# Kernel optimization log

Measured on AMD Instinct MI355X. Metric: run time of the kernel, lower is better.

## Reference

```python
import jax, jax.numpy as jnp
import numpy as np

# dims
T, INPUT_DIM = 128, 512
C_INT, ISQ, DIM, C = 8, 16, 256, 8  # internal_channels, input_square_dim, dim, n_channel
OSQ, OUT_CH = 8, 16                  # output_square_dim, output_size // osq^2
INPUT_SCALE, S1, S2 = 1.0, 0.9, 0.1
K1, D1, K2, D2 = 3, 1, 5, 2


def dw_circ_conv(x, w, dilation):
    """Depthwise conv with circular padding. x: [B,C,H,W], w: [C,1,k,k]."""
    k = w.shape[-1]
    pad = dilation * (k - 1) // 2
    xp = jnp.pad(x, ((0, 0), (0, 0), (pad, pad), (pad, pad)), mode='wrap')
    return jax.lax.conv_general_dilated(
        xp, w, window_strides=(1, 1), padding='VALID',
        rhs_dilation=(dilation, dilation), feature_group_count=x.shape[1])


def setup_inputs() -> dict:
    key = jax.random.key(0)
    ks = jax.random.split(key, 10)
    X = jax.random.normal(ks[0], (T, INPUT_DIM), jnp.float32)
    # nn.Linear weight [out, in]
    W_embed = jax.random.normal(ks[1], (C_INT * ISQ * ISQ, INPUT_DIM), jnp.float32) * 0.02
    mask_coarse = jax.random.bernoulli(ks[2], 0.5, (1, 1, ISQ, ISQ)).astype(jnp.float32)
    mask_fine = jax.random.bernoulli(ks[3], 0.5, (1, 1, DIM, DIM)).astype(jnp.float32)
    # ConvTranspose2d weight [in_ch, out_ch, k, k], k = dim // isq = 16
    W_deconv = jax.random.normal(ks[4], (C_INT, C, DIM // ISQ, DIM // ISQ), jnp.float32) * 0.02

    def lateral_w(k, ksz, p):
        # LateralConnections with conn_exp=1: |w| * bernoulli(p), normalized per output channel
        w = jnp.abs(jax.random.normal(k, (C, 1, ksz, ksz), jnp.float32))
        m = jax.random.bernoulli(jax.random.fold_in(k, 1), p, w.shape).astype(jnp.float32)
        w = w * m
        return w / w.sum(axis=(1, 2, 3), keepdims=True)

    w1 = lateral_w(ks[5], K1, 0.9)
    w2 = lateral_w(ks[6], K2, 0.9)
    # output Conv2d: [out_ch, in_ch, k, k], k = dim // osq = 32
    w_out = jax.random.normal(ks[7], (OUT_CH, C, DIM // OSQ, DIM // OSQ), jnp.float32) * 0.01
    b_out = jax.random.normal(ks[8], (OUT_CH,), jnp.float32) * 0.01
    return dict(X=X, W_embed=W_embed, mask_coarse=mask_coarse, mask_fine=mask_fine,
                W_deconv=W_deconv, w1=w1, w2=w2, w_out=w_out, b_out=b_out)


def reference(X, W_embed, mask_coarse, mask_fine, W_deconv, w1, w2, w_out, b_out):
    t = X.shape[0]
    ksz = W_deconv.shape[-1]
    # CorticalInput
    u = (X @ W_embed.T).reshape(t, C_INT, ISQ, ISQ) * mask_coarse  # [T,Cint,isq,isq]
    # ConvTranspose2d with stride == kernel_size (non-overlapping) == block expansion
    u = jnp.einsum('tcij,coab->toiajb', u, W_deconv).reshape(t, C, ISQ * ksz, ISQ * ksz)
    u = INPUT_SCALE * u * mask_fine  # [T,C,dim,dim]

    # sequential reservoir scan
    def step(Z, x):
        Z = jnp.tanh(S1 * dw_circ_conv(Z, w1, D1) + S2 * dw_circ_conv(Z, w2, D2) + x)
        return Z, Z[0]

    Z0 = jnp.zeros((1, C, DIM, DIM), X.dtype)
    _, outs = jax.lax.scan(step, Z0, u)  # outs: [T,C,dim,dim]

    # readout conv (kernel == stride == dim // osq)
    ko = w_out.shape[-1]
    y = jax.lax.conv_general_dilated(outs, w_out, (ko, ko), 'VALID')
    y = y + b_out[None, :, None, None]
    return y.reshape(t, -1)
```

## Files before the change

### kernel.cpp

```cpp
#include <hip/hip_runtime.h>
#include <math.h>

#define SB_OFF   0
#define E_OFF    524288

typedef float vf4 __attribute__((ext_vector_type(4)));

__device__ __forceinline__ float fast_tanh(float x) {
  x = fminf(fmaxf(x, -15.f), 15.f);
  float ex = __expf(2.f * x);
  return __fdividef(ex - 1.f, ex + 1.f);
}

template <int CTRL>
__device__ __forceinline__ float dpp_add(float v) {
  int x = __builtin_amdgcn_update_dpp(0, __float_as_int(v), CTRL, 0xF, 0xF, true);
  return v + __int_as_float(x);
}

__device__ __forceinline__ void st16(float* p, float a, float b, float c, float d) {
  vf4 v; v.x = a; v.y = b; v.z = c; v.w = d;
  asm volatile("global_store_dwordx4 %0, %1, off sc0 sc1" :: "v"(p), "v"(v) : "memory");
}
__device__ __forceinline__ vf4 ld16(const float* p) {
  vf4 r;
  asm volatile("global_load_dwordx4 %0, %1, off sc0 sc1\n"
               "s_waitcnt vmcnt(0)"
               : "=&v"(r) : "v"(p) : "memory");
  return r;
}
__device__ __forceinline__ void tag_store(unsigned* p, unsigned v) {
  asm volatile("s_waitcnt vmcnt(0)\n"
               "global_store_dword %0, %1, off sc0 sc1" :: "v"(p), "v"(v) : "memory");
}

__global__ __launch_bounds__(256) void prep_kernel(
    const float* __restrict__ X, const float* __restrict__ W_embed,
    const float* __restrict__ mask_coarse, const float* __restrict__ b_out,
    float* __restrict__ ws, float* __restrict__ out)
{
  __shared__ float Xl[128][36];
  __shared__ float Wl[8][36];

  const int tid = threadIdx.x, bid = blockIdx.x;
  float* eb = ws + E_OFF;

  {
    int idx = bid * 512 + tid * 2;
    out[idx]     = b_out[(idx >> 6) & 15];
    out[idx + 1] = b_out[((idx + 1) >> 6) & 15];
  }

  const int o0 = bid * 8;
  const int ol = tid & 7;
  const int tg = tid >> 3;
  float acc[4] = {0.f, 0.f, 0.f, 0.f};

  for (int k0 = 0; k0 < 512; k0 += 32) {
    __syncthreads();
#pragma unroll
    for (int p = 0; p < 4; ++p) {
      int tr = p * 32 + (tid >> 3);
      int kc = (tid & 7) * 4;
      *(float4*)&Xl[tr][kc] = *(const float4*)&X[(size_t)tr * 512 + k0 + kc];
    }
    if (tid < 64) {
      int wr = tid >> 3, wc = (tid & 7) * 4;
      *(float4*)&Wl[wr][wc] = *(const float4*)&W_embed[(size_t)(o0 + wr) * 512 + k0 + wc];
    }
    __syncthreads();
#pragma unroll
    for (int kk = 0; kk < 8; ++kk) {
      float4 w4 = *(const float4*)&Wl[ol][kk * 4];
#pragma unroll
      for (int i = 0; i < 4; ++i) {
        float4 x4 = *(const float4*)&Xl[tg * 4 + i][kk * 4];
        acc[i] = fmaf(w4.x, x4.x, fmaf(w4.y, x4.y, fmaf(w4.z, x4.z, fmaf(w4.w, x4.w, acc[i]))));
      }
    }
  }
  const int o = o0 + ol;
  float mc = mask_coarse[o & 255];
#pragma unroll
  for (int i = 0; i < 4; ++i)
    eb[(size_t)(tg * 4 + i) * 2048 + o] = acc[i] * mc;
}

__global__ __launch_bounds__(512, 2) void scan_kernel(
    const float* __restrict__ mask_fine, const float* __restrict__ W_deconv,
    const float* __restrict__ w1, const float* __restrict__ w2,
    const float* __restrict__ w_out, float* __restrict__ ws,
    float* __restrict__ out)
{
  __shared__ float zin[2][72 * 44];
  __shared__ float rowbuf[2][64 * 17];

  const int tid  = threadIdx.x;
  const int bid  = blockIdx.x;
  const int ch   = bid >> 5;
  const int tile = bid & 31;
  const int tI = tile >> 3, tJ = tile & 7;
  const int r0 = tI << 6, c0 = tJ << 5;
  const int row = tid >> 3;
  const int cg  = tid & 7;
  const int lc  = cg << 2;

  float* Zb = ws + SB_OFF;
  const float* eb = ws + E_OFF;
  const int myoff = (ch * 32 + tile) << 10;

  const int i0 = (r0 + row) >> 4;
  const int jj = (c0 + lc) >> 4;
  float4 wd[8];
#pragma unroll
  for (int c = 0; c < 8; ++c)
    wd[c] = *(const float4*)&W_deconv[(((c * 8 + ch) * 16) + (row & 15)) * 16 + (lc & 15)];
  float4 mf = *(const float4*)&mask_fine[(size_t)(r0 + row) * 256 + c0 + lc];
  float4 wo[16];
#pragma unroll
  for (int oc = 0; oc < 16; ++oc)
    wo[oc] = *(const float4*)&w_out[(((oc * 8 + ch) * 32) + (row & 31)) * 32 + lc];
  float w1s[9], w2s[25];
#pragma unroll
  for (int k = 0; k < 9; ++k)
    w1s[k] = __uint_as_float(__builtin_amdgcn_readfirstlane(__float_as_uint(w1[ch * 9 + k])));
#pragma unroll
  for (int k = 0; k < 25; ++k)
    w2s[k] = __uint_as_float(__builtin_amdgcn_readfirstlane(__float_as_uint(w2[ch * 25 + k])));

  int rd_src = 0, rd_dst = 0, rd_tag = 0;
  const bool hasrd = (tid < 208);
  if (hasrd) {
    int u = tid, di = 0, dj = 0, src = 0, dst = 0, wv = 0;
    if (u < 32) {
      di = -1; src = 128 + (u >> 3) * 32 + (u & 7) * 4;
      dst = (u >> 3) * 44 + 4 + (u & 7) * 4; wv = 7;
    } else if (u < 64) {
      int v = u - 32; di = 1; src = (v >> 3) * 32 + (v & 7) * 4;
      dst = (68 + (v >> 3)) * 44 + 4 + (v & 7) * 4; wv = 0;
    } else if (u < 128) {
      int v = u - 64; dj = -1; src = 512 + v * 4; dst = (4 + v) * 44; wv = v >> 3;
    } else if (u < 192) {
      int v = u - 128; dj = 1; src = 256 + v * 4; dst = (4 + v) * 44 + 36; wv = v >> 3;
    } else {
      int v = u - 192, c = v >> 2, r = v & 3;
      if (c == 0)      { di = -1; dj = -1; src = 816 + r * 4; dst = r * 44;            wv = 7; }
      else if (c == 1) { di = -1; dj = 1;  src = 800 + r * 4; dst = r * 44 + 36;       wv = 7; }
      else if (c == 2) { di = 1;  dj = -1; src = 784 + r * 4; dst = (68 + r) * 44;     wv = 0; }
      else             { di = 1;  dj = 1;  src = 768 + r * 4; dst = (68 + r) * 44 + 36; wv = 0; }
    }
    int nI = (tI + di) & 3, nJ = (tJ + dj) & 7;
    int roff = (ch * 32 + nI * 8 + nJ) << 10;
    rd_src = roff + src;
    rd_tag = roff + 832 + wv * 16;
    rd_dst = dst;
  }

  for (int k = tid; k < 2 * 72 * 44; k += 512) zin[0][k] = 0.f;
  __syncthreads();

  for (int t = 0; t < 128; ++t) {
    float* sb = Zb + (size_t)((t + 1) & 1) * 262144;
    const float* zr = zin[t & 1];
    float*       zw = zin[(t + 1) & 1];
    float*       rb = rowbuf[t & 1];

    float ev[8];
#pragma unroll
    for (int c = 0; c < 8; ++c)
      ev[c] = eb[(size_t)t * 2048 + c * 256 + i0 * 16 + jj];

    float c1a[4] = {0, 0, 0, 0}, c2a[4] = {0, 0, 0, 0};
    {
      float w[12];
      auto load_row = [&](int zrr) {
        float4 A  = *(const float4*)&zr[zrr * 44 + lc];
        float4 B  = *(const float4*)&zr[zrr * 44 + lc + 4];
        float4 Cq = *(const float4*)&zr[zrr * 44 + lc + 8];
        w[0]=A.x; w[1]=A.y; w[2]=A.z; w[3]=A.w;
        w[4]=B.x; w[5]=B.y; w[6]=B.z; w[7]=B.w;
        w[8]=Cq.x; w[9]=Cq.y; w[10]=Cq.z; w[11]=Cq.w;
      };
      auto k2row = [&](int a) {
#pragma unroll
        for (int j = 0; j < 4; ++j)
#pragma unroll
          for (int b = 0; b < 5; ++b)
            c2a[j] = fmaf(w[j + 2 * b], w2s[a * 5 + b], c2a[j]);
      };
      auto k1row = [&](int a) {
#pragma unroll
        for (int j = 0; j < 4; ++j)
#pragma unroll
          for (int b = 0; b < 3; ++b)
            c1a[j] = fmaf(w[j + 3 + b], w1s[a * 3 + b], c1a[j]);
      };
      load_row(row + 0); k2row(0);
      load_row(row + 2); k2row(1);
      load_row(row + 3); k1row(0);
      load_row(row + 4); k1row(1); k2row(2);
      load_row(row + 5); k1row(2);
      load_row(row + 6); k2row(3);
      load_row(row + 8); k2row(4);
    }
    float zv[4];
    {
      const float* mfp = (const float*)&mf;
#pragma unroll
      for (int j = 0; j < 4; ++j) {
        float u = 0.f;
#pragma unroll
        for (int c = 0; c < 8; ++c)
          u = fmaf(ev[c], ((const float*)&wd[c])[j], u);
        float val = fmaf(0.9f, c1a[j], fmaf(0.1f, c2a[j], mfp[j] * u));
        zv[j] = fast_tanh(val);
      }
    }

    if (t < 127) {
      float* rec = sb + myoff;
      if (row < 4)   st16(rec + row * 32 + lc, zv[0], zv[1], zv[2], zv[3]);
      if (row >= 60) st16(rec + 128 + (row - 60) * 32 + lc, zv[0], zv[1], zv[2], zv[3]);
      if (lc == 0)   st16(rec + 256 + row * 4, zv[0], zv[1], zv[2], zv[3]);
      if (lc == 28)  st16(rec + 512 + row * 4, zv[0], zv[1], zv[2], zv[3]);
      if (row < 4 && lc == 0)   st16(rec + 768 + row * 4, zv[0], zv[1], zv[2], zv[3]);
      if (row < 4 && lc == 28)  st16(rec + 784 + row * 4, zv[0], zv[1], zv[2], zv[3]);
      if (row >= 60 && lc == 0) st16(rec + 800 + (row - 60) * 4, zv[0], zv[1], zv[2], zv[3]);
      if (row >= 60 && lc == 28) st16(rec + 816 + (row - 60) * 4, zv[0], zv[1], zv[2], zv[3]);
      if ((tid & 63) == 0)
        tag_store((unsigned*)(rec + 832 + (tid >> 6) * 16), (unsigned)(t + 1));
    }

    *(float4*)&zw[(4 + row) * 44 + 4 + lc] = make_float4(zv[0], zv[1], zv[2], zv[3]);

    float racc[16];
#pragma unroll
    for (int oc = 0; oc < 16; ++oc) {
      const float* wop = (const float*)&wo[oc];
      racc[oc] = fmaf(zv[0], wop[0], fmaf(zv[1], wop[1], fmaf(zv[2], wop[2], zv[3] * wop[3])));
    }
#pragma unroll
    for (int k = 0; k < 16; ++k) {
      racc[k] = dpp_add<0xB1>(racc[k]);
      racc[k] = dpp_add<0x4E>(racc[k]);
      racc[k] = dpp_add<0x141>(racc[k]);
    }
    rb[row * 17 + (cg << 1)]     = racc[cg << 1];
    rb[row * 17 + (cg << 1) + 1] = racc[(cg << 1) + 1];

    if (t < 127 && hasrd) {
      const unsigned tg = (unsigned)(t + 1);
      const unsigned* ta = (const unsigned*)(sb + rd_tag);
      int spins = 0;
      while (__hip_atomic_load(ta, __ATOMIC_RELAXED, __HIP_MEMORY_SCOPE_AGENT) != tg) {
        __builtin_amdgcn_s_sleep(1);
        if (++spins > (1 << 18)) break;
      }
      vf4 v = ld16(sb + rd_src);
      zw[rd_dst]     = v.x;
      zw[rd_dst + 1] = v.y;
      zw[rd_dst + 2] = v.z;
      zw[rd_dst + 3] = v.w;
    }

    __syncthreads();

    if (tid < 32) {
      int p = tid >> 4, oc = tid & 15;
      float s = 0.f;
#pragma unroll
      for (int r = 0; r < 32; ++r) s += rb[(p * 32 + r) * 17 + oc];
      atomicAdd(&out[t * 1024 + oc * 64 + (2 * tI + p) * 8 + tJ], s);
    }
  }
}

extern "C" void kernel_launch(void* const* d_in, const int* in_sizes, int n_in,
                              void* d_out, int out_size, void* d_ws, size_t ws_size,
                              hipStream_t stream) {
  const float* X           = (const float*)d_in[0];
  const float* W_embed     = (const float*)d_in[1];
  const float* mask_coarse = (const float*)d_in[2];
  const float* mask_fine   = (const float*)d_in[3];
  const float* W_deconv    = (const float*)d_in[4];
  const float* w1          = (const float*)d_in[5];
  const float* w2          = (const float*)d_in[6];
  const float* w_out       = (const float*)d_in[7];
  const float* b_out       = (const float*)d_in[8];
  float* ws  = (float*)d_ws;
  float* out = (float*)d_out;

  prep_kernel<<<dim3(256), dim3(256), 0, stream>>>(X, W_embed, mask_coarse, b_out, ws, out);
  scan_kernel<<<dim3(256), dim3(512), 0, stream>>>(mask_fine, W_deconv, w1, w2, w_out, ws, out);
}
```

Baseline: 508.0 us.

## Fuse embedding GEMM prep into scan kernel with a global tag barrier

Removes the separate prep kernel and computes the input-embedding GEMM and bias initialisation at the start of the scan kernel. All blocks then synchronise through per-block tags in workspace before the reservoir scan begins. This is meant to save one kernel launch and the gap between the two kernels. It adds shared memory per block and a spin barrier. The tags are never reset to zero, so on a repeated call the barrier may pass before the embedding data is written.

```diff
diff --git a/kernel.cpp b/kernel.cpp
--- a/kernel.cpp
+++ b/kernel.cpp
@@ -3,6 +3,7 @@
 
 #define SB_OFF   0
 #define E_OFF    524288
+#define PT_OFF   786432
 
 typedef float vf4 __attribute__((ext_vector_type(4)));
 
@@ -21,6 +22,9 @@
 __device__ __forceinline__ void st16(float* p, float a, float b, float c, float d) {
   vf4 v; v.x = a; v.y = b; v.z = c; v.w = d;
   asm volatile("global_store_dwordx4 %0, %1, off sc0 sc1" :: "v"(p), "v"(v) : "memory");
+}
+__device__ __forceinline__ void stc(float* p, float v) {
+  asm volatile("global_store_dword %0, %1, off sc0 sc1" :: "v"(p), "v"(v) : "memory");
 }
 __device__ __forceinline__ vf4 ld16(const float* p) {
   vf4 r;
@@ -34,59 +38,9 @@
                "global_store_dword %0, %1, off sc0 sc1" :: "v"(p), "v"(v) : "memory");
 }
 
-__global__ __launch_bounds__(256) void prep_kernel(
+__global__ __launch_bounds__(512, 2) void scan_kernel(
     const float* __restrict__ X, const float* __restrict__ W_embed,
     const float* __restrict__ mask_coarse, const float* __restrict__ b_out,
-    float* __restrict__ ws, float* __restrict__ out)
-{
-  __shared__ float Xl[128][36];
-  __shared__ float Wl[8][36];
-
-  const int tid = threadIdx.x, bid = blockIdx.x;
-  float* eb = ws + E_OFF;
-
-  {
-    int idx = bid * 512 + tid * 2;
-    out[idx]     = b_out[(idx >> 6) & 15];
-    out[idx + 1] = b_out[((idx + 1) >> 6) & 15];
-  }
-
-  const int o0 = bid * 8;
-  const int ol = tid & 7;
-  const int tg = tid >> 3;
-  float acc[4] = {0.f, 0.f, 0.f, 0.f};
-
-  for (int k0 = 0; k0 < 512; k0 += 32) {
-    __syncthreads();
-#pragma unroll
-    for (int p = 0; p < 4; ++p) {
-      int tr = p * 32 + (tid >> 3);
-      int kc = (tid & 7) * 4;
-      *(float4*)&Xl[tr][kc] = *(const float4*)&X[(size_t)tr * 512 + k0 + kc];
-    }
-    if (tid < 64) {
-      int wr = tid >> 3, wc = (tid & 7) * 4;
-      *(float4*)&Wl[wr][wc] = *(const float4*)&W_embed[(size_t)(o0 + wr) * 512 + k0 + wc];
-    }
-    __syncthreads();
-#pragma unroll
-    for (int kk = 0; kk < 8; ++kk) {
-      float4 w4 = *(const float4*)&Wl[ol][kk * 4];
-#pragma unroll
-      for (int i = 0; i < 4; ++i) {
-        float4 x4 = *(const float4*)&Xl[tg * 4 + i][kk * 4];
-        acc[i] = fmaf(w4.x, x4.x, fmaf(w4.y, x4.y, fmaf(w4.z, x4.z, fmaf(w4.w, x4.w, acc[i]))));
-      }
-    }
-  }
-  const int o = o0 + ol;
-  float mc = mask_coarse[o & 255];
-#pragma unroll
-  for (int i = 0; i < 4; ++i)
-    eb[(size_t)(tg * 4 + i) * 2048 + o] = acc[i] * mc;
-}
-
-__global__ __launch_bounds__(512, 2) void scan_kernel(
     const float* __restrict__ mask_fine, const float* __restrict__ W_deconv,
     const float* __restrict__ w1, const float* __restrict__ w2,
     const float* __restrict__ w_out, float* __restrict__ ws,
@@ -94,9 +48,66 @@
 {
   __shared__ float zin[2][72 * 44];
   __shared__ float rowbuf[2][64 * 17];
+  __shared__ float Xl[128][36];
+  __shared__ float Wl[8][36];
 
   const int tid  = threadIdx.x;
   const int bid  = blockIdx.x;
+  float* Zb = ws + SB_OFF;
+  float* eb = ws + E_OFF;
+  unsigned* ptag = (unsigned*)(ws + PT_OFF);
+
+  {
+    const int ol = tid & 7;
+    const int tg = tid >> 3;
+    float acc0 = 0.f, acc1 = 0.f;
+    for (int k0 = 0; k0 < 512; k0 += 32) {
+      __syncthreads();
+#pragma unroll
+      for (int q = 0; q < 2; ++q) {
+        int u = tid + q * 512;
+        int xr = u >> 3, kc = (u & 7) << 2;
+        *(float4*)&Xl[xr][kc] = *(const float4*)&X[(size_t)xr * 512 + k0 + kc];
+      }
+      if (tid < 64) {
+        int wr = tid >> 3, wc = (tid & 7) << 2;
+        *(float4*)&Wl[wr][wc] = *(const float4*)&W_embed[(size_t)(bid * 8 + wr) * 512 + k0 + wc];
+      }
+      __syncthreads();
+#pragma unroll
+      for (int kk = 0; kk < 8; ++kk) {
+        float4 w4 = *(const float4*)&Wl[ol][kk * 4];
+        float4 x0 = *(const float4*)&Xl[tg * 2 + 0][kk * 4];
+        float4 x1 = *(const float4*)&Xl[tg * 2 + 1][kk * 4];
+        acc0 = fmaf(w4.x, x0.x, fmaf(w4.y, x0.y, fmaf(w4.z, x0.z, fmaf(w4.w, x0.w, acc0))));
+        acc1 = fmaf(w4.x, x1.x, fmaf(w4.y, x1.y, fmaf(w4.z, x1.z, fmaf(w4.w, x1.w, acc1))));
+      }
+    }
+    const int o = bid * 8 + ol;
+    float mc = mask_coarse[o & 255];
+    stc(eb + (size_t)(tg * 2 + 0) * 2048 + o, acc0 * mc);
+    stc(eb + (size_t)(tg * 2 + 1) * 2048 + o, acc1 * mc);
+    if (tid < 128) {
+      int idx = bid * 512 + tid * 4;
+      float b = b_out[(idx >> 6) & 15];
+      st16(out + idx, b, b, b, b);
+    }
+    asm volatile("s_waitcnt vmcnt(0)" ::: "memory");
+    __syncthreads();
+    if (tid == 0) tag_store(ptag + bid * 16, 1u);
+    if (tid < 256) {
+      int spins = 0;
+      while (__hip_atomic_load(ptag + tid * 16, __ATOMIC_RELAXED,
+                               __HIP_MEMORY_SCOPE_AGENT) != 1u) {
+        __builtin_amdgcn_s_sleep(2);
+        if (++spins > (1 << 20)) break;
+      }
+    }
+    __syncthreads();
+    __threadfence();
+    __syncthreads();
+  }
+
   const int ch   = bid >> 5;
   const int tile = bid & 31;
   const int tI = tile >> 3, tJ = tile & 7;
@@ -104,9 +115,6 @@
   const int row = tid >> 3;
   const int cg  = tid & 7;
   const int lc  = cg << 2;
-
-  float* Zb = ws + SB_OFF;
-  const float* eb = ws + E_OFF;
   const int myoff = (ch * 32 + tile) << 10;
 
   const int i0 = (r0 + row) >> 4;
@@ -290,6 +298,6 @@
   float* ws  = (float*)d_ws;
   float* out = (float*)d_out;
 
-  prep_kernel<<<dim3(256), dim3(256), 0, stream>>>(X, W_embed, mask_coarse, b_out, ws, out);
-  scan_kernel<<<dim3(256), dim3(512), 0, stream>>>(mask_fine, W_deconv, w1, w2, w_out, ws, out);
-}
+  scan_kernel<<<dim3(256), dim3(512), 0, stream>>>(
+      X, W_embed, mask_coarse, b_out, mask_fine, W_deconv, w1, w2, w_out, ws, out);
+}
```

New measurement: 534.0 us. 5.1% more time.
